# Optimization experiments

Hardware: AMD Instinct MI355X
Metric: run time of the kernel (lower is better)

Reference implementation:

```python
import jax, jax.numpy as jnp
import numpy as np


def setup_inputs() -> dict:
    key = jax.random.key(0)
    kx, kq, kk, kv = jax.random.split(key, 4)
    B, C, H, W = 4, 512, 64, 64
    CK = C // 8  # low-rank q/k dim
    x = jax.random.normal(kx, (B, C, H, W), dtype=jnp.float32)
    # 1x1 conv weights (spectral-normed at runtime in torch; here plain params,
    # same math: a [out,in] matmul over the flattened spatial dim)
    s = 1.0 / np.sqrt(C)
    Wq = jax.random.normal(kq, (CK, C), dtype=jnp.float32) * s
    Wk = jax.random.normal(kk, (CK, C), dtype=jnp.float32) * s
    Wv = jax.random.normal(kv, (C, C), dtype=jnp.float32) * s
    gamma = jnp.zeros((1,), dtype=jnp.float32)
    return {"x": x, "Wq": Wq, "Wk": Wk, "Wv": Wv, "gamma": gamma}


def reference(x, Wq, Wk, Wv, gamma):
    B, C, H, W = x.shape
    N = H * W
    xf = x.reshape(B, C, N)                         # [B,C,N]
    f = jnp.einsum('kc,bcn->bkn', Wq, xf)           # [B,C/8,N]
    g = jnp.einsum('kc,bcn->bkn', Wk, xf)           # [B,C/8,N]
    h = jnp.einsum('oc,bcn->bon', Wv, xf)           # [B,C,N]
    # scores[b,i,j] = sum_k f[b,k,i] * g[b,k,j]; softmax over dim=1 (i axis)
    scores = jnp.einsum('bki,bkj->bij', f, g)       # [B,N,N]
    beta = jax.nn.softmax(scores, axis=1)
    # o[b,c,j] = sum_i h[b,c,i] * beta[b,i,j]
    o = gamma * jnp.einsum('bci,bij->bcj', h, beta) + xf
    pooled = jnp.mean(o, axis=2).reshape(B, C, 1, 1)  # adaptive_avg_pool2d(.,1)
    return pooled, beta
```

## Files before the change

kernel.cpp:

```cpp
#include <hip/hip_runtime.h>

constexpr int N  = 4096;
constexpr int C  = 512;
constexpr int CK = 64;
constexpr int B  = 4;

typedef __attribute__((ext_vector_type(8))) short short8;
typedef __attribute__((ext_vector_type(4))) float f32x4;

__global__ __launch_bounds__(512, 1)
void proj_fgT(const float* __restrict__ x, const float* __restrict__ Wq,
              const float* __restrict__ Wk,
              ushort* __restrict__ fT_hi, ushort* __restrict__ fT_lo,
              ushort* __restrict__ gT_hi, ushort* __restrict__ gT_lo)
{
    int b  = blockIdx.y;
    int i0 = blockIdx.x * 64;
    __shared__ __align__(16) float  xs[16][64];
    __shared__ __align__(16) float  ws[16][132];
    __shared__ __align__(16) ushort oh[64][136];
    __shared__ __align__(16) ushort ol[64][136];
    int tid = threadIdx.x, ty = tid >> 4, tx = tid & 15;
    float acc[4][4] = {};
    const float* xb = x + (size_t)b * C * N;

    for (int c0 = 0; c0 < C; c0 += 16) {
        if (tid < 256) {
            int cc = tid >> 4, col4 = (tid & 15) * 4;
            *(float4*)&xs[cc][col4] =
                *(const float4*)&xb[(size_t)(c0 + cc) * N + i0 + col4];
        }
        #pragma unroll
        for (int v = tid; v < 2048; v += 512) {
            int row = v >> 4, cc = v & 15;
            ws[cc][row] = (row < 64) ? Wq[row * C + c0 + cc]
                                     : Wk[(row - 64) * C + c0 + cc];
        }
        __syncthreads();
        #pragma unroll
        for (int cc = 0; cc < 16; ++cc) {
            float4 wa = *(const float4*)&ws[cc][ty * 4];
            float4 xa = *(const float4*)&xs[cc][tx * 4];
            float wr[4] = {wa.x, wa.y, wa.z, wa.w};
            float xc[4] = {xa.x, xa.y, xa.z, xa.w};
            #pragma unroll
            for (int r = 0; r < 4; ++r)
                #pragma unroll
                for (int cl = 0; cl < 4; ++cl)
                    acc[r][cl] += wr[r] * xc[cl];
        }
        __syncthreads();
    }

    #pragma unroll
    for (int r = 0; r < 4; ++r)
        #pragma unroll
        for (int cl = 0; cl < 4; ++cl) {
            float v = acc[r][cl];
            unsigned bits = __float_as_uint(v);
            unsigned hb   = bits & 0xFFFF0000u;
            float lof = v - __uint_as_float(hb);
            oh[tx * 4 + cl][ty * 4 + r] = (ushort)(hb >> 16);
            ol[tx * 4 + cl][ty * 4 + r] = (ushort)(__float_as_uint(lof) >> 16);
        }
    __syncthreads();

    int i = tid >> 3, kc = (tid & 7) * 8;
    size_t ofs = ((size_t)b * N + i0 + i) * 64 + kc;
    *(uint4*)&fT_hi[ofs] = *(const uint4*)&oh[i][kc];
    *(uint4*)&fT_lo[ofs] = *(const uint4*)&ol[i][kc];
    *(uint4*)&gT_hi[ofs] = *(const uint4*)&oh[i][64 + kc];
    *(uint4*)&gT_lo[ofs] = *(const uint4*)&ol[i][64 + kc];
}

template <int PASS>
__global__ __launch_bounds__(256, 2)
void scores_pass(const ushort* __restrict__ fT_hi, const ushort* __restrict__ fT_lo,
                 const ushort* __restrict__ gT_hi, const ushort* __restrict__ gT_lo,
                 const float* __restrict__ inv_l, float* __restrict__ colsum,
                 float* __restrict__ beta, float* __restrict__ rowsum)
{
    int b = blockIdx.z, i0 = blockIdx.y * 128, j0 = blockIdx.x * 128;
    __shared__ ushort sm[4][128][72];
    int tid = threadIdx.x;

    const ushort* fh = fT_hi + ((size_t)b * N + i0) * 64;
    const ushort* fl = fT_lo + ((size_t)b * N + i0) * 64;
    const ushort* gh = gT_hi + ((size_t)b * N + j0) * 64;
    const ushort* gl = gT_lo + ((size_t)b * N + j0) * 64;
    #pragma unroll
    for (int v = tid; v < 1024; v += 256) {
        int row = v >> 3, ch = (v & 7) * 8;
        *(uint4*)&sm[0][row][ch] = *(const uint4*)&fh[(size_t)row * 64 + ch];
        *(uint4*)&sm[1][row][ch] = *(const uint4*)&fl[(size_t)row * 64 + ch];
        *(uint4*)&sm[2][row][ch] = *(const uint4*)&gh[(size_t)row * 64 + ch];
        *(uint4*)&sm[3][row][ch] = *(const uint4*)&gl[(size_t)row * 64 + ch];
    }
    __syncthreads();

    int w = tid >> 6, lane = tid & 63, l15 = lane & 15, quad = lane >> 4;
    f32x4 acc[2][8] = {};

    #pragma unroll
    for (int ks = 0; ks < 2; ++ks) {
        int kofs = ks * 32 + quad * 8;
        short8 a_hi[2], a_lo[2];
        #pragma unroll
        for (int tr = 0; tr < 2; ++tr) {
            a_hi[tr] = *(const short8*)&sm[0][w * 32 + tr * 16 + l15][kofs];
            a_lo[tr] = *(const short8*)&sm[1][w * 32 + tr * 16 + l15][kofs];
        }
        #pragma unroll
        for (int tc = 0; tc < 8; ++tc) {
            short8 b_hi = *(const short8*)&sm[2][tc * 16 + l15][kofs];
            short8 b_lo = *(const short8*)&sm[3][tc * 16 + l15][kofs];
            #pragma unroll
            for (int tr = 0; tr < 2; ++tr) {
                acc[tr][tc] = __builtin_amdgcn_mfma_f32_16x16x32_bf16(a_hi[tr], b_hi, acc[tr][tc], 0, 0, 0);
                acc[tr][tc] = __builtin_amdgcn_mfma_f32_16x16x32_bf16(a_hi[tr], b_lo, acc[tr][tc], 0, 0, 0);
                acc[tr][tc] = __builtin_amdgcn_mfma_f32_16x16x32_bf16(a_lo[tr], b_hi, acc[tr][tc], 0, 0, 0);
            }
        }
    }

    if (PASS == 1) {
        float cs[8];
        #pragma unroll
        for (int tc = 0; tc < 8; ++tc) cs[tc] = 0.f;
        #pragma unroll
        for (int tr = 0; tr < 2; ++tr)
            #pragma unroll
            for (int tc = 0; tc < 8; ++tc)
                #pragma unroll
                for (int r = 0; r < 4; ++r)
                    cs[tc] += __expf(acc[tr][tc][r] - 20.0f);
        __syncthreads();
        float* red = (float*)&sm[0][0][0];
        #pragma unroll
        for (int tc = 0; tc < 8; ++tc)
            red[(tc * 16 + l15) * 17 + (w * 4 + quad)] = cs[tc];
        __syncthreads();
        if (tid < 128) {
            float s = 0.f;
            #pragma unroll
            for (int sl = 0; sl < 16; ++sl) s += red[tid * 17 + sl];
            atomicAdd(&colsum[(size_t)b * N + j0 + tid], s);
        }
    } else {
        float il[8];
        #pragma unroll
        for (int tc = 0; tc < 8; ++tc)
            il[tc] = inv_l[(size_t)b * N + j0 + tc * 16 + l15];
        float* pb = beta + (size_t)b * N * N;
        #pragma unroll
        for (int tr = 0; tr < 2; ++tr) {
            float rp[4] = {0.f, 0.f, 0.f, 0.f};
            #pragma unroll
            for (int tc = 0; tc < 8; ++tc) {
                int j = j0 + tc * 16 + l15;
                #pragma unroll
                for (int r = 0; r < 4; ++r) {
                    int i = i0 + w * 32 + tr * 16 + quad * 4 + r;
                    float v = __expf(acc[tr][tc][r] - 20.0f) * il[tc];
                    rp[r] += v;
                    pb[(size_t)i * N + j] = v;
                }
            }
            #pragma unroll
            for (int r = 0; r < 4; ++r) {
                float s = rp[r];
                s += __shfl_xor(s, 1); s += __shfl_xor(s, 2);
                s += __shfl_xor(s, 4); s += __shfl_xor(s, 8);
                if (l15 == 0)
                    atomicAdd(&rowsum[(size_t)b * N + i0 + w * 32 + tr * 16 + quad * 4 + r], s);
            }
        }
    }
}

__global__ __launch_bounds__(256)
void invert_colsum(float* __restrict__ c)
{
    int t = blockIdx.x * 256 + threadIdx.x;
    c[t] = 1.0f / c[t];
}

__global__ __launch_bounds__(256)
void reduce_xr(const float* __restrict__ x, const float* __restrict__ rowsum,
               float* __restrict__ meanx, float* __restrict__ tvec)
{
    int b = blockIdx.y, c = blockIdx.x, tid = threadIdx.x;
    const float* xr = x + ((size_t)b * C + c) * N;
    const float* rr = rowsum + (size_t)b * N;
    float sx = 0.f, st = 0.f;
    for (int base = 0; base < N; base += 1024) {
        int i = base + tid * 4;
        float4 xv = *(const float4*)&xr[i];
        float4 rv = *(const float4*)&rr[i];
        sx += xv.x + xv.y + xv.z + xv.w;
        st += xv.x * rv.x + xv.y * rv.y + xv.z * rv.z + xv.w * rv.w;
    }
    __shared__ float s1[256], s2[256];
    s1[tid] = sx; s2[tid] = st;
    __syncthreads();
    for (int s = 128; s > 0; s >>= 1) {
        if (tid < s) { s1[tid] += s1[tid + s]; s2[tid] += s2[tid + s]; }
        __syncthreads();
    }
    if (tid == 0) {
        meanx[b * C + c] = s1[0] * (1.0f / N);
        tvec [b * C + c] = s2[0];
    }
}

__global__ __launch_bounds__(64)
void pooled_out(const float* __restrict__ Wv, const float* __restrict__ meanx,
                const float* __restrict__ tvec, const float* __restrict__ gamma,
                float* __restrict__ out)
{
    int b = blockIdx.y, c = blockIdx.x;
    const float* wr = Wv + (size_t)c * C;
    const float* t  = tvec + (size_t)b * C;
    float s = 0.f;
    for (int cc = threadIdx.x; cc < C; cc += 64) s += wr[cc] * t[cc];
    for (int off = 32; off > 0; off >>= 1) s += __shfl_down(s, off);
    if (threadIdx.x == 0)
        out[b * C + c] = meanx[b * C + c] + gamma[0] * (1.0f / N) * s;
}

extern "C" void kernel_launch(void* const* d_in, const int* in_sizes, int n_in,
                              void* d_out, int out_size, void* d_ws, size_t ws_size,
                              hipStream_t stream)
{
    const float* x     = (const float*)d_in[0];
    const float* Wq    = (const float*)d_in[1];
    const float* Wk    = (const float*)d_in[2];
    const float* Wv    = (const float*)d_in[3];
    const float* gamma = (const float*)d_in[4];
    float* out  = (float*)d_out;
    float* beta = out + (size_t)B * C;

    ushort* fT_hi = (ushort*)d_ws;
    ushort* fT_lo = fT_hi + (size_t)B * N * 64;
    ushort* gT_hi = fT_lo + (size_t)B * N * 64;
    ushort* gT_lo = gT_hi + (size_t)B * N * 64;
    float*  colsum = (float*)(gT_lo + (size_t)B * N * 64);
    float*  rowsum = colsum + (size_t)B * N;
    float*  meanx  = rowsum + (size_t)B * N;
    float*  tvec   = meanx + (size_t)B * C;

    hipMemsetAsync(colsum, 0, 2 * (size_t)B * N * sizeof(float), stream);

    proj_fgT       <<<dim3(N / 64, B),           512, 0, stream>>>(x, Wq, Wk, fT_hi, fT_lo, gT_hi, gT_lo);
    scores_pass<1> <<<dim3(N / 128, N / 128, B), 256, 0, stream>>>(fT_hi, fT_lo, gT_hi, gT_lo,
                                                                   colsum, colsum, beta, rowsum);
    invert_colsum  <<<dim3(B * N / 256),         256, 0, stream>>>(colsum);
    scores_pass<2> <<<dim3(N / 128, N / 128, B), 256, 0, stream>>>(fT_hi, fT_lo, gT_hi, gT_lo,
                                                                   colsum, colsum, beta, rowsum);
    reduce_xr      <<<dim3(C, B),                256, 0, stream>>>(x, rowsum, meanx, tvec);
    pooled_out     <<<dim3(C, B),                 64, 0, stream>>>(Wv, meanx, tvec, gamma, out);
}
```

Before: 424.7 us.

## Load MFMA operands from global directly and loop blocks over four column tiles

The scores kernel drops its shared-memory staging. Each wave now loads its A fragments (f rows) from global into registers once and keeps them across a loop of four 128-column tiles. B fragments are read straight from global, where they are expected to hit L2/L1. Column-sum reduction now uses wave shuffles and per-wave atomics instead of a shared-memory reduction, and row sums build up across tiles before a single atomic. This removes LDS traffic, barriers and repeated A loads, and quarters the grid. The cost is uncoalesced-ish global fragment reads, more atomics in pass 1, and fewer blocks for latency hiding.

```diff
diff --git a/kernel.cpp b/kernel.cpp
--- a/kernel.cpp
+++ b/kernel.cpp
@@ -80,101 +80,94 @@
                  const float* __restrict__ inv_l, float* __restrict__ colsum,
                  float* __restrict__ beta, float* __restrict__ rowsum)
 {
-    int b = blockIdx.z, i0 = blockIdx.y * 128, j0 = blockIdx.x * 128;
-    __shared__ ushort sm[4][128][72];
+    constexpr int JCHUNK = 512;
+    constexpr int NTILE  = JCHUNK / 128;
+    int b = blockIdx.z, i0 = blockIdx.y * 128, jc0 = blockIdx.x * JCHUNK;
     int tid = threadIdx.x;
-
-    const ushort* fh = fT_hi + ((size_t)b * N + i0) * 64;
-    const ushort* fl = fT_lo + ((size_t)b * N + i0) * 64;
-    const ushort* gh = gT_hi + ((size_t)b * N + j0) * 64;
-    const ushort* gl = gT_lo + ((size_t)b * N + j0) * 64;
+    int w = tid >> 6, lane = tid & 63, l15 = lane & 15, quad = lane >> 4;
+
+    const ushort* fh = fT_hi + ((size_t)b * N + i0 + w * 32 + l15) * 64 + quad * 8;
+    const ushort* fl = fT_lo + ((size_t)b * N + i0 + w * 32 + l15) * 64 + quad * 8;
+    short8 a_hi[2][2], a_lo[2][2];
     #pragma unroll
-    for (int v = tid; v < 1024; v += 256) {
-        int row = v >> 3, ch = (v & 7) * 8;
-        *(uint4*)&sm[0][row][ch] = *(const uint4*)&fh[(size_t)row * 64 + ch];
-        *(uint4*)&sm[1][row][ch] = *(const uint4*)&fl[(size_t)row * 64 + ch];
-        *(uint4*)&sm[2][row][ch] = *(const uint4*)&gh[(size_t)row * 64 + ch];
-        *(uint4*)&sm[3][row][ch] = *(const uint4*)&gl[(size_t)row * 64 + ch];
-    }
-    __syncthreads();
-
-    int w = tid >> 6, lane = tid & 63, l15 = lane & 15, quad = lane >> 4;
-    f32x4 acc[2][8] = {};
-
-    #pragma unroll
-    for (int ks = 0; ks < 2; ++ks) {
-        int kofs = ks * 32 + quad * 8;
-        short8 a_hi[2], a_lo[2];
-        #pragma unroll
-        for (int tr = 0; tr < 2; ++tr) {
-            a_hi[tr] = *(const short8*)&sm[0][w * 32 + tr * 16 + l15][kofs];
-            a_lo[tr] = *(const short8*)&sm[1][w * 32 + tr * 16 + l15][kofs];
-        }
-        #pragma unroll
-        for (int tc = 0; tc < 8; ++tc) {
-            short8 b_hi = *(const short8*)&sm[2][tc * 16 + l15][kofs];
-            short8 b_lo = *(const short8*)&sm[3][tc * 16 + l15][kofs];
-            #pragma unroll
-            for (int tr = 0; tr < 2; ++tr) {
-                acc[tr][tc] = __builtin_amdgcn_mfma_f32_16x16x32_bf16(a_hi[tr], b_hi, acc[tr][tc], 0, 0, 0);
-                acc[tr][tc] = __builtin_amdgcn_mfma_f32_16x16x32_bf16(a_hi[tr], b_lo, acc[tr][tc], 0, 0, 0);
-                acc[tr][tc] = __builtin_amdgcn_mfma_f32_16x16x32_bf16(a_lo[tr], b_hi, acc[tr][tc], 0, 0, 0);
-            }
-        }
-    }
-
-    if (PASS == 1) {
-        float cs[8];
-        #pragma unroll
-        for (int tc = 0; tc < 8; ++tc) cs[tc] = 0.f;
-        #pragma unroll
-        for (int tr = 0; tr < 2; ++tr)
-            #pragma unroll
-            for (int tc = 0; tc < 8; ++tc)
-                #pragma unroll
-                for (int r = 0; r < 4; ++r)
-                    cs[tc] += __expf(acc[tr][tc][r] - 20.0f);
-        __syncthreads();
-        float* red = (float*)&sm[0][0][0];
-        #pragma unroll
-        for (int tc = 0; tc < 8; ++tc)
-            red[(tc * 16 + l15) * 17 + (w * 4 + quad)] = cs[tc];
-        __syncthreads();
-        if (tid < 128) {
-            float s = 0.f;
-            #pragma unroll
-            for (int sl = 0; sl < 16; ++sl) s += red[tid * 17 + sl];
-            atomicAdd(&colsum[(size_t)b * N + j0 + tid], s);
-        }
-    } else {
-        float il[8];
-        #pragma unroll
-        for (int tc = 0; tc < 8; ++tc)
-            il[tc] = inv_l[(size_t)b * N + j0 + tc * 16 + l15];
-        float* pb = beta + (size_t)b * N * N;
-        #pragma unroll
-        for (int tr = 0; tr < 2; ++tr) {
-            float rp[4] = {0.f, 0.f, 0.f, 0.f};
+    for (int tr = 0; tr < 2; ++tr)
+        #pragma unroll
+        for (int ks = 0; ks < 2; ++ks) {
+            a_hi[tr][ks] = *(const short8*)&fh[(size_t)(tr * 16) * 64 + ks * 32];
+            a_lo[tr][ks] = *(const short8*)&fl[(size_t)(tr * 16) * 64 + ks * 32];
+        }
+
+    float rp[2][4] = {};
+
+    #pragma unroll 1
+    for (int jt = 0; jt < NTILE; ++jt) {
+        int j0 = jc0 + jt * 128;
+        const ushort* gh = gT_hi + ((size_t)b * N + j0 + l15) * 64 + quad * 8;
+        const ushort* gl = gT_lo + ((size_t)b * N + j0 + l15) * 64 + quad * 8;
+        f32x4 acc[2][8] = {};
+
+        #pragma unroll
+        for (int ks = 0; ks < 2; ++ks) {
             #pragma unroll
             for (int tc = 0; tc < 8; ++tc) {
-                int j = j0 + tc * 16 + l15;
-                #pragma unroll
-                for (int r = 0; r < 4; ++r) {
-                    int i = i0 + w * 32 + tr * 16 + quad * 4 + r;
-                    float v = __expf(acc[tr][tc][r] - 20.0f) * il[tc];
-                    rp[r] += v;
-                    pb[(size_t)i * N + j] = v;
+                short8 b_hi = *(const short8*)&gh[(size_t)(tc * 16) * 64 + ks * 32];
+                short8 b_lo = *(const short8*)&gl[(size_t)(tc * 16) * 64 + ks * 32];
+                #pragma unroll
+                for (int tr = 0; tr < 2; ++tr) {
+                    acc[tr][tc] = __builtin_amdgcn_mfma_f32_16x16x32_bf16(a_hi[tr][ks], b_hi, acc[tr][tc], 0, 0, 0);
+                    acc[tr][tc] = __builtin_amdgcn_mfma_f32_16x16x32_bf16(a_hi[tr][ks], b_lo, acc[tr][tc], 0, 0, 0);
+                    acc[tr][tc] = __builtin_amdgcn_mfma_f32_16x16x32_bf16(a_lo[tr][ks], b_hi, acc[tr][tc], 0, 0, 0);
                 }
             }
+        }
+
+        if (PASS == 1) {
+            #pragma unroll
+            for (int tc = 0; tc < 8; ++tc) {
+                float s = 0.f;
+                #pragma unroll
+                for (int tr = 0; tr < 2; ++tr)
+                    #pragma unroll
+                    for (int r = 0; r < 4; ++r)
+                        s += __expf(acc[tr][tc][r] - 20.0f);
+                s += __shfl_xor(s, 16);
+                s += __shfl_xor(s, 32);
+                if (lane < 16)
+                    atomicAdd(&colsum[(size_t)b * N + j0 + tc * 16 + l15], s);
+            }
+        } else {
+            float il[8];
+            #pragma unroll
+            for (int tc = 0; tc < 8; ++tc)
+                il[tc] = inv_l[(size_t)b * N + j0 + tc * 16 + l15];
+            float* pb = beta + (size_t)b * N * N;
+            #pragma unroll
+            for (int tr = 0; tr < 2; ++tr)
+                #pragma unroll
+                for (int tc = 0; tc < 8; ++tc) {
+                    int j = j0 + tc * 16 + l15;
+                    #pragma unroll
+                    for (int r = 0; r < 4; ++r) {
+                        int i = i0 + w * 32 + tr * 16 + quad * 4 + r;
+                        float v = __expf(acc[tr][tc][r] - 20.0f) * il[tc];
+                        rp[tr][r] += v;
+                        pb[(size_t)i * N + j] = v;
+                    }
+                }
+        }
+    }
+
+    if (PASS == 2) {
+        #pragma unroll
+        for (int tr = 0; tr < 2; ++tr)
             #pragma unroll
             for (int r = 0; r < 4; ++r) {
-                float s = rp[r];
+                float s = rp[tr][r];
                 s += __shfl_xor(s, 1); s += __shfl_xor(s, 2);
                 s += __shfl_xor(s, 4); s += __shfl_xor(s, 8);
                 if (l15 == 0)
                     atomicAdd(&rowsum[(size_t)b * N + i0 + w * 32 + tr * 16 + quad * 4 + r], s);
             }
-        }
     }
 }
 
@@ -252,10 +245,10 @@
     hipMemsetAsync(colsum, 0, 2 * (size_t)B * N * sizeof(float), stream);
 
     proj_fgT       <<<dim3(N / 64, B),           512, 0, stream>>>(x, Wq, Wk, fT_hi, fT_lo, gT_hi, gT_lo);
-    scores_pass<1> <<<dim3(N / 128, N / 128, B), 256, 0, stream>>>(fT_hi, fT_lo, gT_hi, gT_lo,
+    scores_pass<1> <<<dim3(N / 512, N / 128, B), 256, 0, stream>>>(fT_hi, fT_lo, gT_hi, gT_lo,
                                                                    colsum, colsum, beta, rowsum);
     invert_colsum  <<<dim3(B * N / 256),         256, 0, stream>>>(colsum);
-    scores_pass<2> <<<dim3(N / 128, N / 128, B), 256, 0, stream>>>(fT_hi, fT_lo, gT_hi, gT_lo,
+    scores_pass<2> <<<dim3(N / 512, N / 128, B), 256, 0, stream>>>(fT_hi, fT_lo, gT_hi, gT_lo,
                                                                    colsum, colsum, beta, rowsum);
     reduce_xr      <<<dim3(C, B),                256, 0, stream>>>(x, rowsum, meanx, tvec);
     pooled_out     <<<dim3(C, B),                 64, 0, stream>>>(Wv, meanx, tvec, gamma, out);
```

Measured after the change: 502.6 us. 1.18x slower.

## Replace score recompute pass with single exp pass plus row normalization kernel

Applied to the files above, without the earlier changes.

Scores are now computed once: the kernel writes unnormalized exp values into beta and accumulates column sums. A separate bandwidth-bound kernel then scales each beta row by the inverted column sums and computes row sums, replacing the atomics. This removes the second MFMA recompute of the scores, but it adds a full extra read and write of the large beta matrix.

```diff
diff --git a/kernel.cpp b/kernel.cpp
--- a/kernel.cpp
+++ b/kernel.cpp
@@ -73,12 +73,10 @@
     *(uint4*)&gT_lo[ofs] = *(const uint4*)&ol[i][64 + kc];
 }
 
-template <int PASS>
 __global__ __launch_bounds__(256, 2)
-void scores_pass(const ushort* __restrict__ fT_hi, const ushort* __restrict__ fT_lo,
-                 const ushort* __restrict__ gT_hi, const ushort* __restrict__ gT_lo,
-                 const float* __restrict__ inv_l, float* __restrict__ colsum,
-                 float* __restrict__ beta, float* __restrict__ rowsum)
+void scores_exp(const ushort* __restrict__ fT_hi, const ushort* __restrict__ fT_lo,
+                const ushort* __restrict__ gT_hi, const ushort* __restrict__ gT_lo,
+                float* __restrict__ colsum, float* __restrict__ beta)
 {
     int b = blockIdx.z, i0 = blockIdx.y * 128, j0 = blockIdx.x * 128;
     __shared__ ushort sm[4][128][72];
@@ -123,58 +121,35 @@
         }
     }
 
-    if (PASS == 1) {
-        float cs[8];
-        #pragma unroll
-        for (int tc = 0; tc < 8; ++tc) cs[tc] = 0.f;
-        #pragma unroll
-        for (int tr = 0; tr < 2; ++tr)
-            #pragma unroll
-            for (int tc = 0; tc < 8; ++tc)
-                #pragma unroll
-                for (int r = 0; r < 4; ++r)
-                    cs[tc] += __expf(acc[tr][tc][r] - 20.0f);
-        __syncthreads();
-        float* red = (float*)&sm[0][0][0];
-        #pragma unroll
-        for (int tc = 0; tc < 8; ++tc)
-            red[(tc * 16 + l15) * 17 + (w * 4 + quad)] = cs[tc];
-        __syncthreads();
-        if (tid < 128) {
-            float s = 0.f;
-            #pragma unroll
-            for (int sl = 0; sl < 16; ++sl) s += red[tid * 17 + sl];
-            atomicAdd(&colsum[(size_t)b * N + j0 + tid], s);
-        }
-    } else {
-        float il[8];
-        #pragma unroll
-        for (int tc = 0; tc < 8; ++tc)
-            il[tc] = inv_l[(size_t)b * N + j0 + tc * 16 + l15];
-        float* pb = beta + (size_t)b * N * N;
-        #pragma unroll
-        for (int tr = 0; tr < 2; ++tr) {
-            float rp[4] = {0.f, 0.f, 0.f, 0.f};
-            #pragma unroll
-            for (int tc = 0; tc < 8; ++tc) {
-                int j = j0 + tc * 16 + l15;
-                #pragma unroll
-                for (int r = 0; r < 4; ++r) {
-                    int i = i0 + w * 32 + tr * 16 + quad * 4 + r;
-                    float v = __expf(acc[tr][tc][r] - 20.0f) * il[tc];
-                    rp[r] += v;
-                    pb[(size_t)i * N + j] = v;
-                }
-            }
+    float cs[8];
+    #pragma unroll
+    for (int tc = 0; tc < 8; ++tc) cs[tc] = 0.f;
+    float* pb = beta + (size_t)b * N * N;
+    #pragma unroll
+    for (int tr = 0; tr < 2; ++tr)
+        #pragma unroll
+        for (int tc = 0; tc < 8; ++tc) {
+            int j = j0 + tc * 16 + l15;
             #pragma unroll
             for (int r = 0; r < 4; ++r) {
-                float s = rp[r];
-                s += __shfl_xor(s, 1); s += __shfl_xor(s, 2);
-                s += __shfl_xor(s, 4); s += __shfl_xor(s, 8);
-                if (l15 == 0)
-                    atomicAdd(&rowsum[(size_t)b * N + i0 + w * 32 + tr * 16 + quad * 4 + r], s);
+                int i = i0 + w * 32 + tr * 16 + quad * 4 + r;
+                float v = __expf(acc[tr][tc][r] - 20.0f);
+                cs[tc] += v;
+                pb[(size_t)i * N + j] = v;
             }
         }
+
+    __syncthreads();
+    float* red = (float*)&sm[0][0][0];
+    #pragma unroll
+    for (int tc = 0; tc < 8; ++tc)
+        red[(tc * 16 + l15) * 17 + (w * 4 + quad)] = cs[tc];
+    __syncthreads();
+    if (tid < 128) {
+        float s = 0.f;
+        #pragma unroll
+        for (int sl = 0; sl < 16; ++sl) s += red[tid * 17 + sl];
+        atomicAdd(&colsum[(size_t)b * N + j0 + tid], s);
     }
 }
 
@@ -183,6 +158,32 @@
 {
     int t = blockIdx.x * 256 + threadIdx.x;
     c[t] = 1.0f / c[t];
+}
+
+__global__ __launch_bounds__(256)
+void normalize_rows(const float* __restrict__ inv_l, float* __restrict__ beta,
+                    float* __restrict__ rowsum)
+{
+    int b = blockIdx.y, i = blockIdx.x, tid = threadIdx.x;
+    float* row = beta + ((size_t)b * N + i) * N;
+    const float* il = inv_l + (size_t)b * N;
+    float s = 0.f;
+    #pragma unroll
+    for (int c = 0; c < 4; ++c) {
+        int j = c * 1024 + tid * 4;
+        float4 v = *(float4*)&row[j];
+        float4 l = *(const float4*)&il[j];
+        v.x *= l.x; v.y *= l.y; v.z *= l.z; v.w *= l.w;
+        *(float4*)&row[j] = v;
+        s += v.x + v.y + v.z + v.w;
+    }
+    #pragma unroll
+    for (int off = 32; off > 0; off >>= 1) s += __shfl_down(s, off);
+    __shared__ float wsum[4];
+    if ((tid & 63) == 0) wsum[tid >> 6] = s;
+    __syncthreads();
+    if (tid == 0)
+        rowsum[(size_t)b * N + i] = wsum[0] + wsum[1] + wsum[2] + wsum[3];
 }
 
 __global__ __launch_bounds__(256)
@@ -249,14 +250,13 @@
     float*  meanx  = rowsum + (size_t)B * N;
     float*  tvec   = meanx + (size_t)B * C;
 
-    hipMemsetAsync(colsum, 0, 2 * (size_t)B * N * sizeof(float), stream);
+    hipMemsetAsync(colsum, 0, (size_t)B * N * sizeof(float), stream);
 
     proj_fgT       <<<dim3(N / 64, B),           512, 0, stream>>>(x, Wq, Wk, fT_hi, fT_lo, gT_hi, gT_lo);
-    scores_pass<1> <<<dim3(N / 128, N / 128, B), 256, 0, stream>>>(fT_hi, fT_lo, gT_hi, gT_lo,
-                                                                   colsum, colsum, beta, rowsum);
+    scores_exp     <<<dim3(N / 128, N / 128, B), 256, 0, stream>>>(fT_hi, fT_lo, gT_hi, gT_lo,
+                                                                   colsum, beta);
     invert_colsum  <<<dim3(B * N / 256),         256, 0, stream>>>(colsum);
-    scores_pass<2> <<<dim3(N / 128, N / 128, B), 256, 0, stream>>>(fT_hi, fT_lo, gT_hi, gT_lo,
-                                                                   colsum, colsum, beta, rowsum);
+    normalize_rows <<<dim3(N, B),                256, 0, stream>>>(colsum, beta, rowsum);
     reduce_xr      <<<dim3(C, B),                256, 0, stream>>>(x, rowsum, meanx, tvec);
     pooled_out     <<<dim3(C, B),                 64, 0, stream>>>(Wv, meanx, tvec, gamma, out);
 }
```

Result: slower. 466.2 us (+9.8%).
